# Optimization experiments

Hardware: AMD Instinct MI355X
Metric: run time of the kernel (lower is better)

## Reference

```python
import jax, jax.numpy as jnp
import numpy as np

# MoE config (mirrors init_kwargs)
E = 8        # num_experts
K = 2        # num_experts_per_tok
H = 1024     # hidden_size
F = 2816     # moe_intermediate_size
B, S = 2, 512
NORM_TOPK = True


def setup_inputs() -> dict:
    key = jax.random.key(0)
    ks = jax.random.split(key, 5)
    x = jax.random.normal(ks[0], (B, S, H), dtype=jnp.float32)
    router_w = jax.random.normal(ks[1], (E, H), dtype=jnp.float32) * 0.02   # nn.Linear(H, E).weight
    gate_proj = jax.random.normal(ks[2], (E, H, F), dtype=jnp.float32) * 0.02
    up_proj = jax.random.normal(ks[3], (E, H, F), dtype=jnp.float32) * 0.02
    down_proj = jax.random.normal(ks[4], (E, F, H), dtype=jnp.float32) * 0.02
    return {"x": x, "router_w": router_w, "gate_proj": gate_proj,
            "up_proj": up_proj, "down_proj": down_proj}


def reference(x, router_w, gate_proj, up_proj, down_proj):
    b, s, h = x.shape
    xf = x.reshape(-1, h)                                    # [T, H]
    # Router: softmax over experts, top-k selection mask
    logits = xf @ router_w.T                                 # [T, E]
    probs = jax.nn.softmax(logits, axis=-1)
    topk_p, topk_i = jax.lax.top_k(probs, K)                 # [T, K]
    routing_map = jax.nn.one_hot(topk_i, E, dtype=probs.dtype).sum(axis=1)  # [T, E] 0/1
    if NORM_TOPK:
        probs = probs / topk_p.sum(-1, keepdims=True)
    weight = probs * routing_map                             # [T, E]; zero for unselected experts
    # Per-expert SwiGLU FFN; combine weighted by routing prob.
    # Dense-masked formulation: mathematically identical to the original
    # gather -> per-expert GEMM -> scatter_add, since weight==0 for unrouted pairs.
    g = jnp.einsum('th,ehf->tef', xf, gate_proj)             # [T, E, F]
    u = jnp.einsum('th,ehf->tef', xf, up_proj)               # [T, E, F]
    m = jax.nn.silu(g) * u                                   # [T, E, F]
    out = jnp.einsum('tef,efh,te->th', m, down_proj, weight) # [T, H]
    return out.reshape(b, s, h)
```

## Files before the change

### kernel.cpp

```cpp
#include <hip/hip_runtime.h>

#define HD 1024
#define FD 2816
#define NE 8
#define NT 1024
#define NSLOT (NT * 2)
#define NKT (FD / 32)

typedef short short8 __attribute__((ext_vector_type(8)));
typedef short short4v __attribute__((ext_vector_type(4)));
typedef float f32x2 __attribute__((ext_vector_type(2)));
typedef float f32x4 __attribute__((ext_vector_type(4)));
typedef float f32x16 __attribute__((ext_vector_type(16)));

typedef __attribute__((address_space(3))) unsigned lds_u32;
typedef __attribute__((address_space(1))) const unsigned glb_u32;

__device__ __forceinline__ void glds16(const void* g, void* l) {
  __builtin_amdgcn_global_load_lds((glb_u32*)g, (lds_u32*)l, 16, 0, 0);
}

__device__ __forceinline__ short f2bf(float f) {
  unsigned u = __builtin_bit_cast(unsigned, f);
  u += 0x7FFFu + ((u >> 16) & 1u);
  return (short)(u >> 16);
}
__device__ __forceinline__ int imin(int a, int b) { return a < b ? a : b; }

__global__ void router_kernel(const float* __restrict__ x,
                              const float* __restrict__ rw,
                              int* __restrict__ counts,
                              int* __restrict__ tok_i,
                              float* __restrict__ tok_w) {
  const int t = blockIdx.x;
  const int lane = threadIdx.x;
  const float* px = x + (size_t)t * HD;
  float acc[NE];
#pragma unroll
  for (int e = 0; e < NE; e++) acc[e] = 0.f;
  for (int h = lane; h < HD; h += 64) {
    float xv = px[h];
#pragma unroll
    for (int e = 0; e < NE; e++) acc[e] += xv * rw[e * HD + h];
  }
#pragma unroll
  for (int e = 0; e < NE; e++) {
#pragma unroll
    for (int off = 32; off > 0; off >>= 1)
      acc[e] += __shfl_xor(acc[e], off, 64);
  }
  if (lane == 0) {
    float mx = acc[0];
#pragma unroll
    for (int e = 1; e < NE; e++) mx = fmaxf(mx, acc[e]);
    float ex[NE];
#pragma unroll
    for (int e = 0; e < NE; e++) ex[e] = __expf(acc[e] - mx);
    int i1 = 0;
#pragma unroll
    for (int e = 1; e < NE; e++) if (ex[e] > ex[i1]) i1 = e;
    int i2 = (i1 == 0) ? 1 : 0;
#pragma unroll
    for (int e = 0; e < NE; e++) if (e != i1 && ex[e] > ex[i2]) i2 = e;
    float inv = 1.f / (ex[i1] + ex[i2]);
    tok_i[t * 2 + 0] = i1; tok_w[t * 2 + 0] = ex[i1] * inv;
    tok_i[t * 2 + 1] = i2; tok_w[t * 2 + 1] = ex[i2] * inv;
    atomicAdd(&counts[i1], 1);
    atomicAdd(&counts[i2], 1);
  }
}

__global__ void scan_kernel(const int* __restrict__ counts,
                            int* __restrict__ bases,
                            int* __restrict__ cursor) {
  if (threadIdx.x == 0) {
    int s = 0;
    for (int e = 0; e < NE; e++) { bases[e] = s; cursor[e] = s; s += counts[e]; }
    bases[NE] = s;
  }
}

__global__ void fill_kernel(const int* __restrict__ tok_i,
                            const float* __restrict__ tok_w,
                            int* __restrict__ cursor,
                            int* __restrict__ slot_token,
                            float* __restrict__ slot_w,
                            int* __restrict__ slot_of) {
  int t = blockIdx.x * 256 + threadIdx.x;
  if (t >= NT) return;
#pragma unroll
  for (int k = 0; k < 2; k++) {
    int e = tok_i[t * 2 + k];
    int pos = atomicAdd(&cursor[e], 1);
    slot_token[pos] = t;
    slot_w[pos] = tok_w[t * 2 + k];
    slot_of[t * 2 + k] = pos;
  }
}

__global__ void gather_kernel(const float* __restrict__ x,
                              const int* __restrict__ slot_token,
                              short* __restrict__ xg) {
  const int slot = blockIdx.x;
  const int tok = slot_token[slot];
  const int t = threadIdx.x;
  f32x4 v = *(const f32x4*)(x + (size_t)tok * HD + t * 4);
  short4v s;
#pragma unroll
  for (int j = 0; j < 4; j++) s[j] = f2bf(v[j]);
  *(short4v*)&xg[(size_t)slot * HD + t * 4] = s;
}

__global__ __launch_bounds__(256) void pack_down_kernel(
    const float* __restrict__ dw, short* __restrict__ Pd) {
  const int kt = blockIdx.x, e = blockIdx.y;
  const float* src = dw + (size_t)e * FD * HD + (size_t)kt * 32 * HD;
  short* dst = Pd + ((size_t)e * NKT + kt) * 32768;
  __shared__ short L[8192];
  const int tid = threadIdx.x;
  const int pl = tid & 127, kh = tid >> 7;
  for (int w = 0; w < 4; w++) {
    const int nb = w * 256 + pl * 2;
    f32x2 v[16];
#pragma unroll
    for (int i = 0; i < 16; i++)
      v[i] = *(const f32x2*)(src + (size_t)(kh * 16 + i) * HD + nb);
    if (w) __syncthreads();
#pragma unroll
    for (int ff = 0; ff < 2; ff++)
#pragma unroll
      for (int cc = 0; cc < 2; cc++) {
        int c = kh * 2 + cc;
        short8 s;
#pragma unroll
        for (int q = 0; q < 8; q++) s[q] = f2bf(v[cc * 8 + q][ff]);
        int slot = ((ff << 2) | c) ^ (pl & 7);
        *(short8*)&L[pl * 64 + slot * 8] = s;
      }
    __syncthreads();
#pragma unroll
    for (int j = 0; j < 4; j++) {
      short8 s = *(short8*)&L[j * 2048 + tid * 8];
      *(short8*)&dst[(size_t)w * 8192 + j * 2048 + tid * 8] = s;
    }
  }
}

__global__ __launch_bounds__(256, 2) void gateup_kernel(
    const short* __restrict__ xg, const float* __restrict__ gate_w,
    const float* __restrict__ up_w, const int* __restrict__ bases,
    short* __restrict__ m_out) {
  const int e = blockIdx.z;
  const int b0 = bases[e];
  const int ne = bases[e + 1] - b0;
  const int row0 = blockIdx.y * 128;
  if (row0 >= ne) return;
  const int n0 = blockIdx.x * 64;

  __shared__ short As[2][8192];
  __shared__ short Bs[2][2][4096];

  const int tid = threadIdx.x;
  const int lane = tid & 63, wid = tid >> 6;
  const int l31 = lane & 31, l5 = lane >> 5;
  const int wm = wid >> 1, wn = wid & 1;

  const short* asrc[4];
#pragma unroll
  for (int q = 0; q < 4; q++) {
    int i = q * 256 + tid;
    int sub = i >> 9, ci = i & 511;
    int p = ci >> 3, j = ci & 7;
    int v = j ^ (p & 7);
    int r = 2 * p + (v >> 2), c = v & 3;
    int slot = b0 + imin(row0 + r, ne - 1);
    asrc[q] = xg + (size_t)slot * HD + sub * 32 + c * 8;
  }

  const int mat = tid >> 7;
  const int rb = tid & 127;
  const int fp = rb & 31, kq = rb >> 5;
  const float* wsel = (mat ? up_w : gate_w) + (size_t)e * HD * FD + n0 + fp * 2;

  f32x16 accG[2], accU[2];
#pragma unroll
  for (int fm = 0; fm < 2; fm++) { accG[fm] = (f32x16)0.f; accU[fm] = (f32x16)0.f; }

  f32x2 bv[2][8];

  auto stageA = [&](int buf, int k0) {
#pragma unroll
    for (int q = 0; q < 4; q++)
      glds16(asrc[q] + k0, &As[buf][(q * 256 + wid * 64) * 8]);
  };
  auto loadB = [&](int k0) {
#pragma unroll
    for (int sub = 0; sub < 2; sub++)
#pragma unroll
      for (int i = 0; i < 8; i++)
        bv[sub][i] = *(const f32x2*)(wsel + (size_t)(k0 + sub * 32 + kq * 8 + i) * FD);
  };
  auto writeB = [&](int buf) {
    short* Bd = &Bs[buf][mat][0];
#pragma unroll
    for (int sub = 0; sub < 2; sub++)
#pragma unroll
      for (int ff = 0; ff < 2; ff++) {
        short8 s;
#pragma unroll
        for (int i = 0; i < 8; i++) s[i] = f2bf(bv[sub][i][ff]);
        int slot = ((ff << 2) | kq) ^ (fp & 7);
        *(short8*)&Bd[sub * 2048 + fp * 64 + slot * 8] = s;
      }
  };

  const int NTL = HD / 64;
  stageA(0, 0); loadB(0); writeB(0);
  stageA(1, 64); loadB(64);
  __syncthreads();

  for (int t = 0; t < NTL; t++) {
    const int cur = t & 1;
#pragma unroll
    for (int ks = 0; ks < 4; ks++) {
      const int sub = ks >> 1, chi = (ks & 1) * 2 + l5;
      short8 a[2], bg, bu;
#pragma unroll
      for (int fm = 0; fm < 2; fm++) {
        int r = wm * 64 + fm * 32 + l31;
        int p = r >> 1;
        a[fm] = *(const short8*)&As[cur][sub * 4096 + p * 64 +
                  ((((r & 1) << 2) | chi) ^ (p & 7)) * 8];
      }
      {
        int n = wn * 32 + l31;
        int pn = n >> 1;
        int off = sub * 2048 + pn * 64 + ((((n & 1) << 2) | chi) ^ (pn & 7)) * 8;
        bg = *(const short8*)&Bs[cur][0][off];
        bu = *(const short8*)&Bs[cur][1][off];
      }
#pragma unroll
      for (int fm = 0; fm < 2; fm++) {
        accG[fm] = __builtin_amdgcn_mfma_f32_32x32x16_bf16(a[fm], bg, accG[fm], 0, 0, 0);
        accU[fm] = __builtin_amdgcn_mfma_f32_32x32x16_bf16(a[fm], bu, accU[fm], 0, 0, 0);
      }
    }
    if (t + 1 < NTL) writeB(cur ^ 1);
    __syncthreads();
    if (t + 2 < NTL) { stageA(cur, (t + 2) * 64); loadB((t + 2) * 64); }
  }

#pragma unroll
  for (int fm = 0; fm < 2; fm++)
#pragma unroll
    for (int q = 0; q < 16; q++) {
      int r = row0 + wm * 64 + fm * 32 + (q & 3) + 8 * (q >> 2) + 4 * l5;
      if (r < ne) {
        int slot = b0 + r;
        float g = accG[fm][q], u = accU[fm][q];
        float mv = (g / (1.f + __expf(-g))) * u;
        m_out[(size_t)slot * FD + n0 + wn * 32 + l31] = f2bf(mv);
      }
    }
}

__global__ __launch_bounds__(256, 4) void down_kernel(
    const short* __restrict__ m_in, const short* __restrict__ Pd,
    const int* __restrict__ bases, const float* __restrict__ slot_w,
    float* __restrict__ out_slot) {
  const int e = blockIdx.z;
  const int b0 = bases[e];
  const int ne = bases[e + 1] - b0;
  const int row0 = blockIdx.y * 64;
  if (row0 >= ne) return;
  const int n0 = blockIdx.x * 64;

  __shared__ short As[2][4096];
  __shared__ short Bs[2][4096];

  const int tid = threadIdx.x;
  const int lane = tid & 63, wid = tid >> 6;
  const int l31 = lane & 31, l5 = lane >> 5;
  const int wm = wid >> 1, wn = wid & 1;

  const short* asrc[2];
#pragma unroll
  for (int q = 0; q < 2; q++) {
    int i = q * 256 + tid;
    int sub = i >> 8, ci = i & 255;
    int p = ci >> 3, j = ci & 7;
    int v = j ^ (p & 7);
    int r = 2 * p + (v >> 2), c = v & 3;
    int slot = b0 + imin(row0 + r, ne - 1);
    asrc[q] = m_in + (size_t)slot * FD + sub * 32 + c * 8;
  }
  const short* bbase = Pd + (size_t)e * NKT * 32768 + (size_t)n0 * 32;

  f32x16 acc = (f32x16)0.f;

  auto stage = [&](int buf, int t2) {
    const int k0 = t2 * 64, kt0 = t2 * 2;
#pragma unroll
    for (int q = 0; q < 2; q++) {
      int i = q * 256 + tid;
      int sub = i >> 8, ci = i & 255;
      glds16(asrc[q] + k0, &As[buf][(q * 256 + wid * 64) * 8]);
      glds16(bbase + (size_t)(kt0 + sub) * 32768 + ci * 8,
             &Bs[buf][(q * 256 + wid * 64) * 8]);
    }
  };

  const int NTL = FD / 64;
  stage(0, 0); stage(1, 1);
  __syncthreads();

  for (int t = 0; t < NTL; t++) {
    const int cur = t & 1;
#pragma unroll
    for (int ks = 0; ks < 4; ks++) {
      const int sub = ks >> 1, chi = (ks & 1) * 2 + l5;
      int r = wm * 32 + l31, p = r >> 1;
      short8 a = *(const short8*)&As[cur][sub * 2048 + p * 64 +
                  ((((r & 1) << 2) | chi) ^ (p & 7)) * 8];
      int n = wn * 32 + l31, pn = n >> 1;
      short8 b = *(const short8*)&Bs[cur][sub * 2048 + pn * 64 +
                  ((((n & 1) << 2) | chi) ^ (pn & 7)) * 8];
      acc = __builtin_amdgcn_mfma_f32_32x32x16_bf16(a, b, acc, 0, 0, 0);
    }
    __syncthreads();
    if (t + 2 < NTL) stage(cur, t + 2);
  }

#pragma unroll
  for (int q = 0; q < 16; q++) {
    int r = row0 + wm * 32 + (q & 3) + 8 * (q >> 2) + 4 * l5;
    if (r < ne) {
      int slot = b0 + r;
      out_slot[(size_t)slot * HD + n0 + wn * 32 + l31] = acc[q] * slot_w[slot];
    }
  }
}

__global__ void combine_kernel(const float* __restrict__ out_slot,
                               const int* __restrict__ slot_of,
                               float* __restrict__ out) {
  const int t = blockIdx.x;
  const int s0 = slot_of[t * 2];
  const int s1 = slot_of[t * 2 + 1];
  const int i = threadIdx.x * 4;
  f32x4 a = *(const f32x4*)(out_slot + (size_t)s0 * HD + i);
  f32x4 b = *(const f32x4*)(out_slot + (size_t)s1 * HD + i);
  f32x4 c = a + b;
  *(f32x4*)(out + (size_t)t * HD + i) = c;
}

extern "C" void kernel_launch(void* const* d_in, const int* in_sizes, int n_in,
                              void* d_out, int out_size, void* d_ws,
                              size_t ws_size, hipStream_t stream) {
  const float* x = (const float*)d_in[0];
  const float* rw = (const float*)d_in[1];
  const float* gw = (const float*)d_in[2];
  const float* uw = (const float*)d_in[3];
  const float* dw = (const float*)d_in[4];
  float* out = (float*)d_out;

  char* ws = (char*)d_ws;
  int* counts = (int*)(ws + 0);
  int* cursor = (int*)(ws + 64);
  int* bases = (int*)(ws + 128);
  int* tok_i = (int*)(ws + 256);
  float* tok_w = (float*)(ws + 8448);
  int* slot_token = (int*)(ws + 16640);
  float* slot_w = (float*)(ws + 24832);
  int* slot_of = (int*)(ws + 33024);
  short* xg = (short*)(ws + 41216);
  short* m_buf = (short*)(ws + 4235520);
  float* out_slot = (float*)(ws + 15769856);
  short* Pd = (short*)(ws + 24158464);

  hipMemsetAsync(counts, 0, 64, stream);
  router_kernel<<<NT, 64, 0, stream>>>(x, rw, counts, tok_i, tok_w);
  scan_kernel<<<1, 64, 0, stream>>>(counts, bases, cursor);
  fill_kernel<<<NT / 256, 256, 0, stream>>>(tok_i, tok_w, cursor, slot_token,
                                            slot_w, slot_of);
  gather_kernel<<<NSLOT, 256, 0, stream>>>(x, slot_token, xg);
  pack_down_kernel<<<dim3(NKT, NE), 256, 0, stream>>>(dw, Pd);
  gateup_kernel<<<dim3(FD / 64, 16, NE), 256, 0, stream>>>(xg, gw, uw, bases,
                                                           m_buf);
  down_kernel<<<dim3(HD / 64, 32, NE), 256, 0, stream>>>(m_buf, Pd, bases,
                                                         slot_w, out_slot);
  combine_kernel<<<NT, 256, 0, stream>>>(out_slot, slot_of, out);
}
```

Measured before the change: 210.4 us.

## Restructure MoE GEMM pipelines with explicit waitcnt, triple buffering and wider B loads

The gate/up kernel now loads B weights as float4 instead of float2 and double-buffers them in registers. It waits on vmcnt explicitly and uses raw barriers, so global loads overlap MFMA work instead of draining at every __syncthreads. The down kernel moves to a three-stage LDS ring with partial vmcnt waits, and its occupancy bound drops from 4 to 3 to make room for the extra LDS. Both grids are flattened so expert and N-tile come from blockIdx.x, which changes block scheduling order. Hand-written waitcnt counts carry a correctness risk if the in-flight load counts are wrong.

```diff
diff --git a/kernel.cpp b/kernel.cpp
--- a/kernel.cpp
+++ b/kernel.cpp
@@ -15,6 +15,9 @@
 
 typedef __attribute__((address_space(3))) unsigned lds_u32;
 typedef __attribute__((address_space(1))) const unsigned glb_u32;
+
+#define WAITV(N) asm volatile("s_waitcnt vmcnt(" #N ") lgkmcnt(0)" ::: "memory")
+#define BARRIER() do { __builtin_amdgcn_s_barrier(); __builtin_amdgcn_sched_barrier(0); } while (0)
 
 __device__ __forceinline__ void glds16(const void* g, void* l) {
   __builtin_amdgcn_global_load_lds((glb_u32*)g, (lds_u32*)l, 16, 0, 0);
@@ -150,12 +153,13 @@
     const short* __restrict__ xg, const float* __restrict__ gate_w,
     const float* __restrict__ up_w, const int* __restrict__ bases,
     short* __restrict__ m_out) {
-  const int e = blockIdx.z;
+  const int bx = blockIdx.x;
+  const int e = bx / 44, nt = bx - e * 44;
   const int b0 = bases[e];
   const int ne = bases[e + 1] - b0;
   const int row0 = blockIdx.y * 128;
   if (row0 >= ne) return;
-  const int n0 = blockIdx.x * 64;
+  const int n0 = nt * 64;
 
   __shared__ short As[2][8192];
   __shared__ short Bs[2][2][4096];
@@ -179,48 +183,39 @@
 
   const int mat = tid >> 7;
   const int rb = tid & 127;
-  const int fp = rb & 31, kq = rb >> 5;
-  const float* wsel = (mat ? up_w : gate_w) + (size_t)e * HD * FD + n0 + fp * 2;
+  const int fp2 = rb & 15, kq2 = rb >> 4;
+  const float* wsel = (mat ? up_w : gate_w) + (size_t)e * HD * FD + n0 + fp2 * 4;
 
   f32x16 accG[2], accU[2];
 #pragma unroll
   for (int fm = 0; fm < 2; fm++) { accG[fm] = (f32x16)0.f; accU[fm] = (f32x16)0.f; }
 
-  f32x2 bv[2][8];
+  f32x4 bvA[8], bvB[8];
 
   auto stageA = [&](int buf, int k0) {
 #pragma unroll
     for (int q = 0; q < 4; q++)
       glds16(asrc[q] + k0, &As[buf][(q * 256 + wid * 64) * 8]);
   };
-  auto loadB = [&](int k0) {
-#pragma unroll
-    for (int sub = 0; sub < 2; sub++)
-#pragma unroll
-      for (int i = 0; i < 8; i++)
-        bv[sub][i] = *(const f32x2*)(wsel + (size_t)(k0 + sub * 32 + kq * 8 + i) * FD);
-  };
-  auto writeB = [&](int buf) {
+  auto loadB = [&](f32x4 (&bv)[8], int k0) {
+#pragma unroll
+    for (int i = 0; i < 8; i++)
+      bv[i] = *(const f32x4*)(wsel + (size_t)(k0 + kq2 * 8 + i) * FD);
+  };
+  auto writeB = [&](int buf, f32x4 (&bv)[8]) {
     short* Bd = &Bs[buf][mat][0];
-#pragma unroll
-    for (int sub = 0; sub < 2; sub++)
-#pragma unroll
-      for (int ff = 0; ff < 2; ff++) {
-        short8 s;
-#pragma unroll
-        for (int i = 0; i < 8; i++) s[i] = f2bf(bv[sub][i][ff]);
-        int slot = ((ff << 2) | kq) ^ (fp & 7);
-        *(short8*)&Bd[sub * 2048 + fp * 64 + slot * 8] = s;
-      }
-  };
-
-  const int NTL = HD / 64;
-  stageA(0, 0); loadB(0); writeB(0);
-  stageA(1, 64); loadB(64);
-  __syncthreads();
-
-  for (int t = 0; t < NTL; t++) {
-    const int cur = t & 1;
+    const int sub = kq2 >> 2, c = kq2 & 3;
+#pragma unroll
+    for (int ff = 0; ff < 4; ff++) {
+      int fl = fp2 * 4 + ff, p = fl >> 1;
+      int j = (((fl & 1) << 2) | c) ^ (p & 7);
+      short8 s;
+#pragma unroll
+      for (int i = 0; i < 8; i++) s[i] = f2bf(bv[i][ff]);
+      *(short8*)&Bd[sub * 2048 + p * 64 + j * 8] = s;
+    }
+  };
+  auto mfma_on = [&](int cur) {
 #pragma unroll
     for (int ks = 0; ks < 4; ks++) {
       const int sub = ks >> 1, chi = (ks & 1) * 2 + l5;
@@ -232,23 +227,46 @@
         a[fm] = *(const short8*)&As[cur][sub * 4096 + p * 64 +
                   ((((r & 1) << 2) | chi) ^ (p & 7)) * 8];
       }
-      {
-        int n = wn * 32 + l31;
-        int pn = n >> 1;
-        int off = sub * 2048 + pn * 64 + ((((n & 1) << 2) | chi) ^ (pn & 7)) * 8;
-        bg = *(const short8*)&Bs[cur][0][off];
-        bu = *(const short8*)&Bs[cur][1][off];
-      }
+      int n = wn * 32 + l31, pn = n >> 1;
+      int off = sub * 2048 + pn * 64 + ((((n & 1) << 2) | chi) ^ (pn & 7)) * 8;
+      bg = *(const short8*)&Bs[cur][0][off];
+      bu = *(const short8*)&Bs[cur][1][off];
 #pragma unroll
       for (int fm = 0; fm < 2; fm++) {
         accG[fm] = __builtin_amdgcn_mfma_f32_32x32x16_bf16(a[fm], bg, accG[fm], 0, 0, 0);
         accU[fm] = __builtin_amdgcn_mfma_f32_32x32x16_bf16(a[fm], bu, accU[fm], 0, 0, 0);
       }
     }
-    if (t + 1 < NTL) writeB(cur ^ 1);
-    __syncthreads();
-    if (t + 2 < NTL) { stageA(cur, (t + 2) * 64); loadB((t + 2) * 64); }
-  }
+  };
+
+  stageA(0, 0);
+  loadB(bvA, 0);
+  stageA(1, 64);
+  writeB(0, bvA);
+  loadB(bvA, 64);
+  WAITV(12);
+  BARRIER();
+
+  for (int tp = 0; tp < 14; tp += 2) {
+    loadB(bvB, (tp + 2) * 64);
+    mfma_on(0);
+    writeB(1, bvA);
+    WAITV(8);
+    BARRIER();
+    stageA(0, (tp + 2) * 64);
+
+    loadB(bvA, (tp + 3) * 64);
+    mfma_on(1);
+    writeB(0, bvB);
+    WAITV(8);
+    BARRIER();
+    stageA(1, (tp + 3) * 64);
+  }
+  mfma_on(0);
+  writeB(1, bvA);
+  WAITV(0);
+  BARRIER();
+  mfma_on(1);
 
 #pragma unroll
   for (int fm = 0; fm < 2; fm++)
@@ -264,19 +282,19 @@
     }
 }
 
-__global__ __launch_bounds__(256, 4) void down_kernel(
+__global__ __launch_bounds__(256, 3) void down_kernel(
     const short* __restrict__ m_in, const short* __restrict__ Pd,
     const int* __restrict__ bases, const float* __restrict__ slot_w,
     float* __restrict__ out_slot) {
-  const int e = blockIdx.z;
+  const int bx = blockIdx.x;
+  const int e = bx >> 4, nt = bx & 15;
   const int b0 = bases[e];
   const int ne = bases[e + 1] - b0;
   const int row0 = blockIdx.y * 64;
   if (row0 >= ne) return;
-  const int n0 = blockIdx.x * 64;
-
-  __shared__ short As[2][4096];
-  __shared__ short Bs[2][4096];
+
+  __shared__ short As[3][4096];
+  __shared__ short Bs[3][4096];
 
   const int tid = threadIdx.x;
   const int lane = tid & 63, wid = tid >> 6;
@@ -294,49 +312,62 @@
     int slot = b0 + imin(row0 + r, ne - 1);
     asrc[q] = m_in + (size_t)slot * FD + sub * 32 + c * 8;
   }
-  const short* bbase = Pd + (size_t)e * NKT * 32768 + (size_t)n0 * 32;
+  const short* bbase = Pd + (size_t)e * NKT * 32768 + (size_t)nt * 2048;
 
   f32x16 acc = (f32x16)0.f;
 
-  auto stage = [&](int buf, int t2) {
+  auto stage = [&](short* Ab, short* Bb, int t2) {
     const int k0 = t2 * 64, kt0 = t2 * 2;
 #pragma unroll
     for (int q = 0; q < 2; q++) {
       int i = q * 256 + tid;
       int sub = i >> 8, ci = i & 255;
-      glds16(asrc[q] + k0, &As[buf][(q * 256 + wid * 64) * 8]);
-      glds16(bbase + (size_t)(kt0 + sub) * 32768 + ci * 8,
-             &Bs[buf][(q * 256 + wid * 64) * 8]);
-    }
-  };
-
-  const int NTL = FD / 64;
-  stage(0, 0); stage(1, 1);
-  __syncthreads();
-
-  for (int t = 0; t < NTL; t++) {
-    const int cur = t & 1;
+      glds16(asrc[q] + k0, Ab + i * 8);
+      glds16(bbase + (size_t)(kt0 + sub) * 32768 + ci * 8, Bb + i * 8);
+    }
+  };
+  auto compute = [&](const short* Ab, const short* Bb) {
 #pragma unroll
     for (int ks = 0; ks < 4; ks++) {
       const int sub = ks >> 1, chi = (ks & 1) * 2 + l5;
       int r = wm * 32 + l31, p = r >> 1;
-      short8 a = *(const short8*)&As[cur][sub * 2048 + p * 64 +
-                  ((((r & 1) << 2) | chi) ^ (p & 7)) * 8];
+      short8 a = *(const short8*)(Ab + sub * 2048 + p * 64 +
+                  ((((r & 1) << 2) | chi) ^ (p & 7)) * 8);
       int n = wn * 32 + l31, pn = n >> 1;
-      short8 b = *(const short8*)&Bs[cur][sub * 2048 + pn * 64 +
-                  ((((n & 1) << 2) | chi) ^ (pn & 7)) * 8];
+      short8 b = *(const short8*)(Bb + sub * 2048 + pn * 64 +
+                  ((((n & 1) << 2) | chi) ^ (pn & 7)) * 8);
       acc = __builtin_amdgcn_mfma_f32_32x32x16_bf16(a, b, acc, 0, 0, 0);
     }
-    __syncthreads();
-    if (t + 2 < NTL) stage(cur, t + 2);
-  }
+  };
+
+  const int NTL = FD / 64;
+  short *a0 = As[0], *a1 = As[1], *a2 = As[2];
+  short *bb0 = Bs[0], *bb1 = Bs[1], *bb2 = Bs[2];
+
+  stage(a0, bb0, 0);
+  stage(a1, bb1, 1);
+  WAITV(4);
+  BARRIER();
+
+  for (int t = 0; t < NTL - 2; ++t) {
+    stage(a2, bb2, t + 2);
+    compute(a0, bb0);
+    WAITV(4);
+    BARRIER();
+    short* ta = a0; a0 = a1; a1 = a2; a2 = ta;
+    short* tb = bb0; bb0 = bb1; bb1 = bb2; bb2 = tb;
+  }
+  compute(a0, bb0);
+  WAITV(0);
+  BARRIER();
+  compute(a1, bb1);
 
 #pragma unroll
   for (int q = 0; q < 16; q++) {
     int r = row0 + wm * 32 + (q & 3) + 8 * (q >> 2) + 4 * l5;
     if (r < ne) {
       int slot = b0 + r;
-      out_slot[(size_t)slot * HD + n0 + wn * 32 + l31] = acc[q] * slot_w[slot];
+      out_slot[(size_t)slot * HD + nt * 64 + wn * 32 + l31] = acc[q] * slot_w[slot];
     }
   }
 }
@@ -385,9 +416,8 @@
                                             slot_w, slot_of);
   gather_kernel<<<NSLOT, 256, 0, stream>>>(x, slot_token, xg);
   pack_down_kernel<<<dim3(NKT, NE), 256, 0, stream>>>(dw, Pd);
-  gateup_kernel<<<dim3(FD / 64, 16, NE), 256, 0, stream>>>(xg, gw, uw, bases,
-                                                           m_buf);
-  down_kernel<<<dim3(HD / 64, 32, NE), 256, 0, stream>>>(m_buf, Pd, bases,
-                                                         slot_w, out_slot);
+  gateup_kernel<<<dim3(352, 16), 256, 0, stream>>>(xg, gw, uw, bases, m_buf);
+  down_kernel<<<dim3(128, 32), 256, 0, stream>>>(m_buf, Pd, bases, slot_w,
+                                                 out_slot);
   combine_kernel<<<NT, 256, 0, stream>>>(out_slot, slot_of, out);
 }
```

After: 201.3 us. -4.3%, faster.
